# Optimization experiments

Hardware: AMD Instinct MI355X
Metric: run time of the kernel (lower is better)

Reference implementation:

```python
import jax, jax.numpy as jnp
import numpy as np

B, N = 32, 2048
SLOTS, PSD, VIEW = 5, 15, 9
DM, NH, MH, EGO = 64, 4, 128, 32
PAIR_D = SLOTS * (SLOTS - 1) // 2          # 10
TER_D = VIEW * VIEW                        # 81
NBR_D = SLOTS * PSD + PAIR_D               # 85
D_OBS = EGO + NBR_D + TER_D                # 198


def setup_inputs() -> dict:
    key = jax.random.key(0)
    ks = jax.random.split(key, 64)

    def _p(k, shape, s=0.05):
        return (jax.random.normal(k, shape) * s).astype(jnp.float32)

    def z(*shape):
        return jnp.zeros(shape, jnp.float32)

    # --- observation with some genuinely-masked slots (r == 0) ---
    ego = jax.random.normal(ks[0], (B, N, EGO), jnp.float32)
    nbr = jax.random.normal(ks[1], (B, N, SLOTS, PSD), jnp.float32)
    keep = jax.random.bernoulli(ks[2], 0.8, (B, N, SLOTS)).astype(jnp.float32)
    nbr = jnp.concatenate([nbr[..., 0:3] * keep[..., None], nbr[..., 3:]], axis=-1)
    pair = jax.random.normal(ks[3], (B, N, PAIR_D), jnp.float32)
    ter = jax.random.normal(ks[4], (B, N, TER_D), jnp.float32)
    obs = jnp.concatenate([ego, nbr.reshape(B, N, SLOTS * PSD), pair, ter], axis=-1)

    i = 5
    def nk():
        nonlocal i
        i += 1
        return ks[i - 1]

    params = {
        "tok_w": _p(nk(), (12, DM)), "tok_b": z(DM),
        "ln1_s": jnp.ones((DM,), jnp.float32), "ln1_b": z(DM),
        "a1_qw": _p(nk(), (DM, DM)), "a1_qb": z(DM),
        "a1_kw": _p(nk(), (DM, DM)), "a1_kb": z(DM),
        "a1_vw": _p(nk(), (DM, DM)), "a1_vb": z(DM),
        "a1_ow": _p(nk(), (DM, DM)), "a1_ob": z(DM),
        "ln2_s": jnp.ones((DM,), jnp.float32), "ln2_b": z(DM),
        "m1_w": _p(nk(), (DM, MH)), "m1_b": z(MH),
        "m2_w": _p(nk(), (MH, MH)), "m2_b": z(MH),
        "m3_w": _p(nk(), (MH, DM)), "m3_b": z(DM),
        "e1_w": _p(nk(), (EGO, MH)), "e1_b": z(MH),
        "e2_w": _p(nk(), (MH, MH)), "e2_b": z(MH),
        "e3_w": _p(nk(), (MH, DM)), "e3_b": z(DM),
        "l1_w": _p(nk(), (2 * DM, MH)), "l1_b": z(MH),
        "l2_w": _p(nk(), (MH, MH)), "l2_b": z(MH),
        "l3_w": _p(nk(), (MH, 1)), "l3_b": z(1),
        "seed": _p(nk(), (1, 1, DM), 0.02),
        "p_qw": _p(nk(), (DM, DM)), "p_qb": z(DM),
        "p_kw": _p(nk(), (DM, DM)), "p_kb": z(DM),
        "p_vw": _p(nk(), (DM, DM)), "p_vb": z(DM),
        "p_ow": _p(nk(), (DM, DM)), "p_ob": z(DM),
        "pr_w": _p(nk(), (PAIR_D, DM)), "pr_b": z(DM),
        "h1_w": _p(nk(), (EGO + 2 * DM, MH)), "h1_b": z(MH),
        "h2_w": _p(nk(), (MH, MH)), "h2_b": z(MH),
        "h3_w": _p(nk(), (MH, MH)), "h3_b": z(MH),
    }
    return {"obs": obs, **params}


def _layernorm(x, s, b, eps=1e-6):
    m = jnp.mean(x, axis=-1, keepdims=True)
    v = jnp.var(x, axis=-1, keepdims=True)
    return (x - m) * jax.lax.rsqrt(v + eps) * s + b


def _zero_if_masked(x, mask):
    return jnp.where(mask[..., None], x, jnp.array(0.0, x.dtype))


def _masked_softmax(logits, mask, eps=1e-9):
    mask = mask.astype(bool)
    very_neg = jnp.array(-1e9, logits.dtype)
    ml = jnp.where(mask, logits, very_neg)
    mx = jnp.max(ml, axis=-1, keepdims=True)
    ex = jnp.exp(ml - mx) * mask.astype(logits.dtype)
    return ex / (jnp.sum(ex, axis=-1, keepdims=True) + eps)


def _mha(q_in, kv_in, attn_mask, qw, qb, kw, kb, vw, vb, ow, ob, nh=NH):
    dm = q_in.shape[-1]
    dh = dm // nh
    q = (q_in @ qw + qb).reshape(*q_in.shape[:-1], nh, dh)
    k = (kv_in @ kw + kb).reshape(*kv_in.shape[:-1], nh, dh)
    v = (kv_in @ vw + vb).reshape(*kv_in.shape[:-1], nh, dh)
    logits = jnp.einsum('...qhd,...khd->...hqk', q, k) / jnp.sqrt(jnp.float32(dh))
    neg = jnp.finfo(logits.dtype).min
    logits = jnp.where(attn_mask, logits, neg)
    attn = jax.nn.softmax(logits, axis=-1)
    o = jnp.einsum('...hqk,...khd->...qhd', attn, v).reshape(*q_in.shape[:-1], dm)
    return o @ ow + ob


def _mlp3(x, w1, b1, w2, b2, w3, b3):
    x = jax.nn.gelu(x @ w1 + b1)
    x = jax.nn.gelu(x @ w2 + b2)
    return x @ w3 + b3


def reference(obs, tok_w, tok_b, ln1_s, ln1_b,
              a1_qw, a1_qb, a1_kw, a1_kb, a1_vw, a1_vb, a1_ow, a1_ob,
              ln2_s, ln2_b, m1_w, m1_b, m2_w, m2_b, m3_w, m3_b,
              e1_w, e1_b, e2_w, e2_b, e3_w, e3_b,
              l1_w, l1_b, l2_w, l2_b, l3_w, l3_b,
              seed, p_qw, p_qb, p_kw, p_kb, p_vw, p_vb, p_ow, p_ob,
              pr_w, pr_b, h1_w, h1_b, h2_w, h2_b, h3_w, h3_b):
    obs = obs.astype(jnp.float32)
    Bb, Nn, Dd = obs.shape
    ego = obs[..., :EGO]
    nbr_all = obs[..., EGO:EGO + NBR_D]
    nbr_main = nbr_all[..., :SLOTS * PSD].reshape(Bb, Nn, SLOTS, PSD)
    pair = nbr_all[..., SLOTS * PSD:]

    r = nbr_main[..., 0:3]
    u = nbr_main[..., 3:6]
    att = nbr_main[..., 6:9]
    fre = nbr_main[..., 9:10]
    tem = nbr_main[..., 10:11]
    inv = nbr_main[..., 11:15]

    mask = jnp.any(jnp.abs(r) > 1e-6, axis=-1)                 # (B,N,K)
    mask_any = jnp.any(mask, axis=-1, keepdims=True)           # (B,N,1)
    mask_safe = jnp.where(mask_any, mask, mask.at[..., 0].set(True))

    r_clean = jnp.nan_to_num(r, nan=0.0, posinf=0.0, neginf=0.0)
    diff = r_clean[..., :, None, :] - r_clean[..., None, :, :]
    dist = jnp.linalg.norm(diff, axis=-1)                      # (B,N,K,K)
    pair_mask = mask[..., :, None] & mask[..., None, :]
    eye = jnp.eye(SLOTS, dtype=bool)[None, None]
    valid = pair_mask & ~eye
    big = jnp.array(1e9, dist.dtype)
    dist_no_self = jnp.where(eye, big, dist)
    d_min = jnp.min(jnp.where(valid, dist_no_self, big), axis=-1, keepdims=True)
    d_sum = jnp.sum(jnp.where(valid, dist, 0.0), axis=-1, keepdims=True)
    cnt = jnp.sum(valid, axis=-1, keepdims=True).astype(dist.dtype)
    d_mean = jnp.where(cnt > 0, d_sum / (cnt + 1e-9), 0.0)
    att_norm = jnp.linalg.norm(att, axis=-1, keepdims=True)

    tok_in = jnp.concatenate([inv, fre, tem, att, att_norm, d_min, d_mean], axis=-1)  # (B,N,K,12)
    tok = jax.nn.gelu(tok_in @ tok_w + tok_b)
    tok = _zero_if_masked(tok, mask)

    # --- SetTransformerBlock ---
    qk = mask_safe[..., :, None] & mask_safe[..., None, :]
    attn_mask = qk[..., None, :, :]                            # (B,N,1,K,K)
    y = _layernorm(tok, ln1_s, ln1_b)
    y = _mha(y, y, attn_mask, a1_qw, a1_qb, a1_kw, a1_kb, a1_vw, a1_vb, a1_ow, a1_ob)
    y = _zero_if_masked(y, mask)
    tok = tok + y
    zz = _layernorm(tok, ln2_s, ln2_b)
    zz = _mlp3(zz, m1_w, m1_b, m2_w, m2_b, m3_w, m3_b)
    zz = _zero_if_masked(zz, mask)
    tok = _zero_if_masked(tok + zz, mask)

    # --- alpha weights ---
    ego_ctx = _mlp3(ego, e1_w, e1_b, e2_w, e2_b, e3_w, e3_b)   # (B,N,DM)
    ego_ctx_b = jnp.broadcast_to(ego_ctx[..., None, :], tok.shape)
    logits = _mlp3(jnp.concatenate([tok, ego_ctx_b], axis=-1),
                   l1_w, l1_b, l2_w, l2_b, l3_w, l3_b)[..., 0]
    alpha = _masked_softmax(logits, mask)
    alpha3 = alpha[..., None]
    v_r = jnp.sum(alpha3 * r, axis=-2)
    v_u = jnp.sum(alpha3 * u, axis=-2)

    # --- AttentionPool ---
    q = jnp.broadcast_to(seed, (*tok.shape[:-2], 1, DM)).astype(jnp.float32)
    pool_mask = mask_safe[..., None, None, :]                  # (B,N,1,1,K)
    c = _mha(q, tok, pool_mask, p_qw, p_qb, p_kw, p_kb, p_vw, p_vb, p_ow, p_ob)[..., 0, :]
    c = jnp.where(mask_any, c, jnp.zeros_like(c))

    pair_emb = jax.nn.gelu(pair @ pr_w + pr_b)
    h_in = jnp.concatenate([ego, c, pair_emb], axis=-1)
    h = _mlp3(h_in, h1_w, h1_b, h2_w, h2_b, h3_w, h3_b)
    return jnp.concatenate([h, v_r, v_u], axis=-1)             # (B,N,134)
```

## Files before the change

### kernel.cpp

```cpp
#include <hip/hip_runtime.h>
#include <math.h>


#define DOBS 198
#define NEG_INF_F (-3.402823466e38f)

#define BAR() do { asm volatile("s_waitcnt lgkmcnt(0)" ::: "memory"); \
                   __builtin_amdgcn_s_barrier(); } while(0)

typedef __bf16 v8bf __attribute__((ext_vector_type(8)));
typedef __bf16 v4bf __attribute__((ext_vector_type(4)));
typedef float  v4f  __attribute__((ext_vector_type(4)));

struct P {
  const float *obs,*tok_w,*tok_b,*ln1_s,*ln1_b,
    *a1_qw,*a1_qb,*a1_kw,*a1_kb,*a1_vw,*a1_vb,*a1_ow,*a1_ob,
    *ln2_s,*ln2_b,*m1_w,*m1_b,*m2_w,*m2_b,*m3_w,*m3_b,
    *e1_w,*e1_b,*e2_w,*e2_b,*e3_w,*e3_b,
    *l1_w,*l1_b,*l2_w,*l2_b,*l3_w,*l3_b,
    *seed,*p_qw,*p_qb,*p_kw,*p_kb,*p_vw,*p_vb,*p_ow,*p_ob,
    *pr_w,*pr_b,*h1_w,*h1_b,*h2_w,*h2_b,*h3_w,*h3_b;
  float* out;
};
static_assert(sizeof(P) == 51*sizeof(void*), "P layout");

#define W_A1Q 0
#define W_A1K 4096
#define W_A1V 8192
#define W_A1O 12288
#define W_M1  16384
#define W_M2  24576
#define W_M3  40960
#define W_E1  49152
#define W_E2  53248
#define W_E3  69632
#define W_L1  77824
#define W_L2  94208
#define W_PK  110592
#define W_PV  114688
#define W_PO  118784
#define W_H1  122880
#define W_H2  143360
#define W_H3  159744
#define W_END 176128
#define W_QP  176128

__global__ __launch_bounds__(256)
void prep_w(P a, __bf16* ws)
{
  if (blockIdx.x == 172){
    int t = threadIdx.x;
    if (t < 64){
      float acc = a.p_qb[t];
      for (int k=0;k<64;k++) acc += a.seed[k]*a.p_qw[k*64+t];
      ((float*)(ws + W_QP))[t] = acc;
    }
    return;
  }
  const float* srcs[18] = {a.a1_qw,a.a1_kw,a.a1_vw,a.a1_ow,a.m1_w,a.m2_w,a.m3_w,
                           a.e1_w,a.e2_w,a.e3_w,a.l1_w,a.l2_w,a.p_kw,a.p_vw,a.p_ow,
                           a.h1_w,a.h2_w,a.h3_w};
  const int Ks[18]   = {64,64,64,64,64,128,128,32,128,128,128,128,64,64,64,160,128,128};
  const int Ns[18]   = {64,64,64,64,128,128,64,128,128,64,128,128,64,64,64,128,128,128};
  const int offs[18] = {W_A1Q,W_A1K,W_A1V,W_A1O,W_M1,W_M2,W_M3,W_E1,W_E2,W_E3,
                        W_L1,W_L2,W_PK,W_PV,W_PO,W_H1,W_H2,W_H3};
  __shared__ float tile[32][33];
  int b = blockIdx.x, m = 0, acc = 0;
  for (; m < 18; m++){
    int t = (Ks[m]/32)*(Ns[m]/32);
    if (b < acc + t) break;
    acc += t;
  }
  int lt = b - acc, K = Ks[m], N = Ns[m];
  int ntile = N/32, kt = lt/ntile, nt = lt%ntile;
  int tx = threadIdx.x & 31, ty = threadIdx.x >> 5;
  const float* S = srcs[m];
  #pragma unroll
  for (int rr=0; rr<32; rr+=8)
    tile[ty+rr][tx] = S[(size_t)(kt*32+ty+rr)*N + nt*32+tx];
  __syncthreads();
  __bf16* D = ws + offs[m];
  #pragma unroll
  for (int rr=0; rr<32; rr+=8)
    D[(size_t)(nt*32+ty+rr)*K + kt*32+tx] = (__bf16)tile[tx][ty+rr];
}

__device__ __forceinline__ float gelu_f(float x){
  float t = x * fmaf(0.0356774081f, x*x, 0.7978845608f);
  float u = __builtin_amdgcn_exp2f(-2.885390082f * t);
  return x * __builtin_amdgcn_rcpf(1.0f + u);
}

__device__ __forceinline__ void load16f(const __bf16* p, float* f){
  v8bf a = *(const v8bf*)p, b = *(const v8bf*)(p+8);
  #pragma unroll
  for (int i=0;i<8;i++){ f[i]=(float)a[i]; f[8+i]=(float)b[i]; }
}

template<int KT,int NTPW> struct WF {
  v8bf  w[NTPW][KT];
  float4 b[NTPW];
};

template<int KT,int NTPW>
__device__ __forceinline__ WF<KT,NTPW> wload(const __bf16* __restrict__ Wt,
    const float* __restrict__ bias, int wv, int lane)
{
  WF<KT,NTPW> f;
  const int ar = lane&15, quad = lane>>4;
  #pragma unroll
  for (int ln=0; ln<NTPW; ln++){
    const int wt = wv*NTPW + ln;
    const __bf16* wp = Wt + (size_t)(wt*16+ar)*(KT*32) + quad*8;
    #pragma unroll
    for (int kt=0;kt<KT;kt++) f.w[ln][kt] = *(const v8bf*)(wp + kt*32);
    f.b[ln] = *(const float4*)(bias + wt*16 + quad*4);
  }
  return f;
}

template<int KT,int MT,int NTPW,typename LA,typename E>
__device__ __forceinline__ void gemmW(LA la, const WF<KT,NTPW>& f,
    int wv, int lane, E epi)
{
  const int ar = lane&15, quad = lane>>4;
  #pragma unroll
  for (int ln=0; ln<NTPW; ln++){
    const int wt = wv*NTPW + ln;
    #pragma unroll
    for (int mt=0; mt<MT; mt++){
      v4f c; c[0]=f.b[ln].x; c[1]=f.b[ln].y; c[2]=f.b[ln].z; c[3]=f.b[ln].w;
      #pragma unroll
      for (int kt=0;kt<KT;kt++)
        c = __builtin_amdgcn_mfma_f32_16x16x32_bf16(f.w[ln][kt], la(mt,kt,ar,quad), c, 0,0,0);
      epi(wt*16 + quad*4, mt, ar, c);
    }
  }
}

__global__ __launch_bounds__(256,3)
void swarm_mfma(P a, const __bf16* __restrict__ ws, int ntok)
{
  __shared__ char smem[53120] __attribute__((aligned(16)));
  __bf16* Ab   = (__bf16*)(smem);
  __bf16* Bb   = (__bf16*)(smem+17408);
  float*  TOKIN= (float*) (smem+17408);
  __bf16* Tk   = (__bf16*)(smem+34816);
  float*  OBSf = (float*) (smem+34816);
  __bf16* Po   = (__bf16*)(smem+34816);
  __bf16* Pe   = (__bf16*)(smem+44032);
  __bf16* Eg   = (__bf16*)(smem+46080);
  __bf16* Ru   = (__bf16*)(smem+47360);
  __bf16* mfb  = (__bf16*)(smem+48096);
  __bf16* msfb = (__bf16*)(smem+48224);
  float*  many = (float*) (smem+48352);
  float*  lga  = (float*) (smem+48416);
  __bf16* ECX  = (__bf16*)(smem+48672);
  float*  pattn= (float*) (smem+48672);
  __bf16* ATTb = (__bf16*)(smem+50720);
  __bf16* Cc   = (__bf16*)(smem+50720);

  const int lane = threadIdx.x & 63;
  const int wv   = threadIdx.x >> 6;
  const int ar   = lane & 15, quad = lane >> 4;
  const long blkT0 = (long)blockIdx.x*12;

  for (int it=lane; it<3*117; it+=64){
    int tg=it/117, c=it-tg*117;
    long gt = blkT0 + 3*wv + tg; if (gt>ntok-1) gt=ntok-1;
    OBSf[(3*wv+tg)*120+c] = a.obs[gt*DOBS+c];
  }
  float* Df = (float*)Ab;
  for (int it=lane; it<75; it+=64){
    int tg=it/25, p=it-tg*25, i=p/5, j=p-i*5;
    const float* ob = OBSf + (3*wv+tg)*120 + 32;
    float d2=0.f;
    #pragma unroll
    for (int d=0;d<3;d++){
      float ri=ob[15*i+d]; ri = isfinite(ri)?ri:0.f;
      float rj=ob[15*j+d]; rj = isfinite(rj)?rj:0.f;
      float df=ri-rj; d2 += df*df;
    }
    Df[(3*wv+tg)*32+p]=sqrtf(d2);
  }
  if (lane<15){
    int T=3*wv+lane/5, s=lane%5;
    const float* b = OBSf + T*120 + 32 + 15*s;
    mfb[15*wv+lane] = (__bf16)((fabsf(b[0])>1e-6f||fabsf(b[1])>1e-6f||fabsf(b[2])>1e-6f)?1.f:0.f);
  }
  if (wv==0 && lane>=60){ mfb[lane]=(__bf16)0.f; msfb[lane]=(__bf16)0.f; }
  if (wv==0 && lane>=12 && lane<16) many[lane]=0.f;
  if (lane<3){
    int T=3*wv+lane;
    float any = (float)mfb[T*5]+(float)mfb[T*5+1]+(float)mfb[T*5+2]+(float)mfb[T*5+3]+(float)mfb[T*5+4];
    float anyf = (any>0.f)?1.f:0.f; many[T]=anyf;
    #pragma unroll
    for (int i=0;i<5;i++) msfb[T*5+i] = (anyf>0.f)? mfb[T*5+i] : (__bf16)((i==0)?1.f:0.f);
  }
  if (lane<15){
    int T=3*wv+lane/5, i=lane%5, R=15*wv+lane;
    float dmin=1e9f,dsum=0.f,cnt=0.f;
    #pragma unroll
    for (int j=0;j<5;j++){
      if (j!=i && (float)mfb[T*5+i]>0.5f && (float)mfb[T*5+j]>0.5f){
        float dd=Df[T*32+i*5+j];
        dmin=fminf(dmin,dd); dsum+=dd; cnt+=1.f;
      }
    }
    TOKIN[R*12+10]=dmin;
    TOKIN[R*12+11]=(cnt>0.f)? dsum/(cnt+1e-9f) : 0.f;
  }
  for (int it=lane; it<150; it+=64){
    int tg=it/50, q=it-tg*50, s=q/10, c=q-s*10;
    int T=3*wv+tg;
    const float* b = OBSf + T*120 + 32 + 15*s;
    float v;
    if (c<4)        v=b[11+c];
    else if (c==4)  v=b[9];
    else if (c==5)  v=b[10];
    else if (c<9)   v=b[6+(c-6)];
    else { float a0=b[6],a1=b[7],a2=b[8]; v=sqrtf(a0*a0+a1*a1+a2*a2); }
    TOKIN[(T*5+s)*12+c]=v;
  }
  for (int it=lane; it<96; it+=64){
    int tg=it>>5, c=it&31;
    Eg[(3*wv+tg)*40+c] = (__bf16)OBSf[(3*wv+tg)*120+c];
  }
  for (int it=lane; it<90; it+=64){
    int tg=it/30, c=it-tg*30;
    Ru[(3*wv+tg)*30+c] = (__bf16)OBSf[(3*wv+tg)*120+32+15*(c/6)+(c%6)];
  }
  for (int it=lane; it<192; it+=64){
    int tg=it>>6, c=it&63;
    float acc = a.pr_b[c];
    #pragma unroll
    for (int k=0;k<10;k++) acc += OBSf[(3*wv+tg)*120+107+k]*a.pr_w[k*64+c];
    Pe[(3*wv+tg)*64+c] = (__bf16)gelu_f(acc);
  }
  BAR();

  auto wfK = wload<2,1>(ws+W_A1K, a.a1_kb, wv, lane);

  {
    float w0[12];
    #pragma unroll
    for (int k=0;k<12;k++) w0[k] = a.tok_w[k*64+lane];
    float tb = a.tok_b[lane];
    for (int r=0;r<15;r++){
      int R = 15*wv + r;
      const float4* tin = (const float4*)(TOKIN + R*12);
      float4 x0 = tin[0], x1 = tin[1], x2 = tin[2];
      float acc = tb;
      acc=fmaf(x0.x,w0[0],acc); acc=fmaf(x0.y,w0[1],acc);
      acc=fmaf(x0.z,w0[2],acc); acc=fmaf(x0.w,w0[3],acc);
      acc=fmaf(x1.x,w0[4],acc); acc=fmaf(x1.y,w0[5],acc);
      acc=fmaf(x1.z,w0[6],acc); acc=fmaf(x1.w,w0[7],acc);
      acc=fmaf(x2.x,w0[8],acc); acc=fmaf(x2.y,w0[9],acc);
      acc=fmaf(x2.z,w0[10],acc); acc=fmaf(x2.w,w0[11],acc);
      Tk[R*72+lane] = (__bf16)(gelu_f(acc)*(float)mfb[R]);
    }
  }
  if (ar<15){
    int R = 15*wv + ar;
    float x[16]; load16f(Tk + R*72 + quad*16, x);
    float s=0.f;
    #pragma unroll
    for (int i=0;i<16;i++) s += x[i];
    s += __shfl_xor(s,16,64); s += __shfl_xor(s,32,64);
    float m = s*(1.f/64.f), q=0.f;
    #pragma unroll
    for (int i=0;i<16;i++){ float d=x[i]-m; q=fmaf(d,d,q); }
    q += __shfl_xor(q,16,64); q += __shfl_xor(q,32,64);
    float rs = __builtin_amdgcn_rsqf(q*(1.f/64.f)+1e-6f);
    v8bf o0,o1;
    #pragma unroll
    for (int i=0;i<8;i++){
      o0[i]=(__bf16)((x[i]  -m)*rs*a.ln1_s[quad*16+i]  +a.ln1_b[quad*16+i]);
      o1[i]=(__bf16)((x[8+i]-m)*rs*a.ln1_s[quad*16+8+i]+a.ln1_b[quad*16+8+i]);
    }
    *(v8bf*)(Ab+R*136+quad*16)=o0; *(v8bf*)(Ab+R*136+quad*16+8)=o1;
  }
  BAR();

  auto actAb = [&](int mt,int kt,int r,int q){ return *(const v8bf*)(Ab + (size_t)(mt*16+r)*136 + q*8 + kt*32); };
  auto actBb = [&](int mt,int kt,int r,int q){ return *(const v8bf*)(Bb + (size_t)(mt*16+r)*136 + q*8 + kt*32); };
  auto actTk = [&](int mt,int kt,int r,int q){ return *(const v8bf*)(Tk + (size_t)(mt*16+r)*72  + q*8 + kt*32); };

  auto wfV = wload<2,1>(ws+W_A1V, a.a1_vb, wv, lane);
  auto wfQ = wload<2,1>(ws+W_A1Q, a.a1_qb, wv, lane);
  gemmW<2,4,1>(actAb, wfK, wv, lane,
    [&](int wb,int mt,int r,v4f c){ v4bf o;
      #pragma unroll
      for (int k=0;k<4;k++) o[k]=(__bf16)c[k];
      *(v4bf*)&Bb[(mt*16+r)*136+64+wb]=o; });
  gemmW<2,4,1>(actAb, wfV, wv, lane,
    [&](int wb,int mt,int r,v4f c){ v4bf o;
      #pragma unroll
      for (int k=0;k<4;k++) o[k]=(__bf16)c[k];
      *(v4bf*)&Ab[(mt*16+r)*136+64+wb]=o; });
  gemmW<2,4,1>(actAb, wfQ, wv, lane,
    [&](int wb,int mt,int r,v4f c){ v4bf o;
      #pragma unroll
      for (int k=0;k<4;k++) o[k]=(__bf16)c[k];
      *(v4bf*)&Bb[(mt*16+r)*136+wb]=o; });
  auto wfO = wload<2,1>(ws+W_A1O, a.a1_ob, wv, lane);
  BAR();

  if (lane<60){
    int tg=lane/20, rem=lane-tg*20, h=rem/5, i=rem-h*5;
    int T=3*wv+tg;
    bool mi = (float)msfb[T*5+i]>0.5f;
    float qv[16]; load16f(&Bb[(T*5+i)*136 + h*16], qv);
    float lgv[5], mx=NEG_INF_F;
    #pragma unroll
    for (int j=0;j<5;j++){
      float kk[16]; load16f(&Bb[(T*5+j)*136 + 64 + h*16], kk);
      float d=0.f;
      #pragma unroll
      for (int dd=0;dd<16;dd++) d += qv[dd]*kk[dd];
      bool mj = (float)msfb[T*5+j]>0.5f;
      lgv[j] = (mi&&mj)? d*0.25f : NEG_INF_F;
      mx = fmaxf(mx,lgv[j]);
    }
    float sum=0.f, ex[5];
    #pragma unroll
    for (int j=0;j<5;j++){ ex[j]=__expf(lgv[j]-mx); sum+=ex[j]; }
    float inv=1.0f/sum;
    #pragma unroll
    for (int j=0;j<5;j++) ATTb[T*100+(h*5+i)*5+j]=(__bf16)(ex[j]*inv);
  }
  {
    int h = lane>>4;
    #pragma unroll
    for (int tg=0; tg<3; tg++){
      int T=3*wv+tg;
      float v5[5];
      #pragma unroll
      for (int j=0;j<5;j++) v5[j] = (float)Ab[(T*5+j)*136+64+lane];
      #pragma unroll
      for (int i=0;i<5;i++){
        float o=0.f;
        #pragma unroll
        for (int j=0;j<5;j++) o += (float)ATTb[T*100+(h*5+i)*5+j]*v5[j];
        Ab[(T*5+i)*136+lane]=(__bf16)o;
      }
    }
  }
  BAR();

  gemmW<2,4,1>(actAb, wfO, wv, lane,
    [&](int wb,int mt,int r,v4f c){
      int R=mt*16+r; float mm=(float)mfb[R];
      v4bf old=*(const v4bf*)&Tk[R*72+wb]; v4bf o;
      #pragma unroll
      for (int k=0;k<4;k++) o[k]=(__bf16)((float)old[k]+c[k]*mm);
      *(v4bf*)&Tk[R*72+wb]=o; });
  auto wfM1 = wload<2,2>(ws+W_M1, a.m1_b, wv, lane);
  BAR();

  if (ar<15){
    int R = 15*wv + ar;
    float x[16]; load16f(Tk + R*72 + quad*16, x);
    float s=0.f;
    #pragma unroll
    for (int i=0;i<16;i++) s += x[i];
    s += __shfl_xor(s,16,64); s += __shfl_xor(s,32,64);
    float m = s*(1.f/64.f), q=0.f;
    #pragma unroll
    for (int i=0;i<16;i++){ float d=x[i]-m; q=fmaf(d,d,q); }
    q += __shfl_xor(q,16,64); q += __shfl_xor(q,32,64);
    float rs = __builtin_amdgcn_rsqf(q*(1.f/64.f)+1e-6f);
    v8bf o0,o1;
    #pragma unroll
    for (int i=0;i<8;i++){
      o0[i]=(__bf16)((x[i]  -m)*rs*a.ln2_s[quad*16+i]  +a.ln2_b[quad*16+i]);
      o1[i]=(__bf16)((x[8+i]-m)*rs*a.ln2_s[quad*16+8+i]+a.ln2_b[quad*16+8+i]);
    }
    *(v8bf*)(Ab+R*136+quad*16)=o0; *(v8bf*)(Ab+R*136+quad*16+8)=o1;
  }
  BAR();

  gemmW<2,4,2>(actAb, wfM1, wv, lane,
    [&](int wb,int mt,int r,v4f c){ v4bf o;
      #pragma unroll
      for (int k=0;k<4;k++) o[k]=(__bf16)gelu_f(c[k]);
      *(v4bf*)&Bb[(mt*16+r)*136+wb]=o; });
  auto wfM2 = wload<4,2>(ws+W_M2, a.m2_b, wv, lane);
  BAR();
  gemmW<4,4,2>(actBb, wfM2, wv, lane,
    [&](int wb,int mt,int r,v4f c){ v4bf o;
      #pragma unroll
      for (int k=0;k<4;k++) o[k]=(__bf16)gelu_f(c[k]);
      *(v4bf*)&Ab[(mt*16+r)*136+wb]=o; });
  auto wfM3 = wload<4,1>(ws+W_M3, a.m3_b, wv, lane);
  auto wfE1 = wload<1,2>(ws+W_E1, a.e1_b, wv, lane);
  BAR();
  gemmW<4,4,1>(actAb, wfM3, wv, lane,
    [&](int wb,int mt,int r,v4f c){
      int R=mt*16+r; float mm=(float)mfb[R];
      v4bf old=*(const v4bf*)&Tk[R*72+wb]; v4bf o;
      #pragma unroll
      for (int k=0;k<4;k++) o[k]=(__bf16)(((float)old[k]+c[k]*mm)*mm);
      *(v4bf*)&Tk[R*72+wb]=o; });
  gemmW<1,1,2>([&](int,int,int r,int q){ return *(const v8bf*)(Eg + (size_t)r*40 + q*8); },
    wfE1, wv, lane,
    [&](int wb,int mt,int r,v4f c){ v4bf o;
      #pragma unroll
      for (int k=0;k<4;k++) o[k]=(__bf16)gelu_f(c[k]);
      *(v4bf*)&Bb[r*136+wb]=o; });
  auto wfE2 = wload<4,2>(ws+W_E2, a.e2_b, wv, lane);
  BAR();
  gemmW<4,1,2>(actBb, wfE2, wv, lane,
    [&](int wb,int mt,int r,v4f c){ v4bf o;
      #pragma unroll
      for (int k=0;k<4;k++) o[k]=(__bf16)gelu_f(c[k]);
      *(v4bf*)&Ab[r*136+wb]=o; });
  auto wfE3 = wload<4,1>(ws+W_E3, a.e3_b, wv, lane);
  BAR();
  gemmW<4,1,1>(actAb, wfE3, wv, lane,
    [&](int wb,int mt,int r,v4f c){ v4bf o;
      #pragma unroll
      for (int k=0;k<4;k++) o[k]=(__bf16)c[k];
      *(v4bf*)&ECX[r*64+wb]=o; });
  auto wfL1 = wload<4,2>(ws+W_L1, a.l1_b, wv, lane);
  BAR();
  gemmW<4,4,2>([&](int mt,int kt,int r,int q){
      int R=mt*16+r;
      return (kt<2) ? *(const v8bf*)(Tk + (size_t)R*72 + q*8 + kt*32)
                    : *(const v8bf*)(ECX + (size_t)((R*205)>>10)*64 + q*8 + (kt-2)*32); },
    wfL1, wv, lane,
    [&](int wb,int mt,int r,v4f c){ v4bf o;
      #pragma unroll
      for (int k=0;k<4;k++) o[k]=(__bf16)gelu_f(c[k]);
      *(v4bf*)&Bb[(mt*16+r)*136+wb]=o; });
  auto wfL2 = wload<4,2>(ws+W_L2, a.l2_b, wv, lane);
  BAR();
  gemmW<4,4,2>(actBb, wfL2, wv, lane,
    [&](int wb,int mt,int r,v4f c){ v4bf o;
      #pragma unroll
      for (int k=0;k<4;k++) o[k]=(__bf16)gelu_f(c[k]);
      *(v4bf*)&Ab[(mt*16+r)*136+wb]=o; });
  auto wfPK = wload<2,1>(ws+W_PK, a.p_kb, wv, lane);
  auto wfPV = wload<2,1>(ws+W_PV, a.p_vb, wv, lane);
  BAR();

  if (ar<15){
    int R = 15*wv + ar;
    float x[16], y[16];
    load16f(&Ab[R*136 + quad*32], x);
    load16f(&Ab[R*136 + quad*32 + 16], y);
    const float* w = a.l3_w + quad*32;
    float p = 0.f;
    #pragma unroll
    for (int i=0;i<16;i++) p = fmaf(x[i], w[i], p);
    #pragma unroll
    for (int i=0;i<16;i++) p = fmaf(y[i], w[16+i], p);
    p += __shfl_xor(p,16,64); p += __shfl_xor(p,32,64);
    if (quad==0) lga[R] = p + a.l3_b[0];
  }
  gemmW<2,4,1>(actTk, wfPK, wv, lane,
    [&](int wb,int mt,int r,v4f c){ v4bf o;
      #pragma unroll
      for (int k=0;k<4;k++) o[k]=(__bf16)c[k];
      *(v4bf*)&Bb[(mt*16+r)*136+wb]=o; });
  gemmW<2,4,1>(actTk, wfPV, wv, lane,
    [&](int wb,int mt,int r,v4f c){ v4bf o;
      #pragma unroll
      for (int k=0;k<4;k++) o[k]=(__bf16)c[k];
      *(v4bf*)&Bb[(mt*16+r)*136+64+wb]=o; });
  if (lane<3){
    int T=3*wv+lane;
    float ml[5], mx=-1e9f;
    #pragma unroll
    for (int i=0;i<5;i++){ ml[i]=((float)mfb[T*5+i]>0.5f)? lga[T*5+i] : -1e9f; mx=fmaxf(mx,ml[i]); }
    float den=0.f, e[5];
    #pragma unroll
    for (int i=0;i<5;i++){ e[i]=__expf(ml[i]-mx)*(float)mfb[T*5+i]; den+=e[i]; }
    float inv=1.0f/(den+1e-9f);
    #pragma unroll
    for (int i=0;i<5;i++) lga[T*5+i]=e[i]*inv;
  }
  if (lane<18){
    int tg=lane/6, c=lane-tg*6;
    int T=3*wv+tg;
    float v=0.f;
    #pragma unroll
    for (int i=0;i<5;i++) v += lga[T*5+i]*(float)Ru[T*30+i*6+c];
    long tk = blkT0 + T;
    if (tk<ntok) a.out[tk*134+128+c]=v;
  }
  BAR();

  if (lane<12){
    const float* qg = (const float*)(ws + W_QP);
    int tg=lane>>2, h=lane&3;
    int T=3*wv+tg;
    float qv[16];
    #pragma unroll
    for (int dd=0;dd<16;dd++) qv[dd]=qg[h*16+dd];
    float lgv[5], mx=NEG_INF_F;
    #pragma unroll
    for (int j=0;j<5;j++){
      float kk[16]; load16f(&Bb[(T*5+j)*136 + h*16], kk);
      float d=0.f;
      #pragma unroll
      for (int dd=0;dd<16;dd++) d += qv[dd]*kk[dd];
      lgv[j] = ((float)msfb[T*5+j]>0.5f)? d*0.25f : NEG_INF_F;
      mx = fmaxf(mx,lgv[j]);
    }
    float sum=0.f, ex[5];
    #pragma unroll
    for (int j=0;j<5;j++){ ex[j]=__expf(lgv[j]-mx); sum+=ex[j]; }
    float inv=1.0f/sum;
    #pragma unroll
    for (int j=0;j<5;j++) pattn[T*20+h*5+j]=ex[j]*inv;
  }
  for (int it=lane; it<192; it+=64){
    int tg=it>>6, c=it&63, h=c>>4;
    int T=3*wv+tg;
    float o=0.f;
    #pragma unroll
    for (int j=0;j<5;j++)
      o += pattn[T*20+h*5+j]*(float)Bb[(T*5+j)*136+64+c];
    Po[T*64+c]=(__bf16)o;
  }
  auto wfPO = wload<2,1>(ws+W_PO, a.p_ob, wv, lane);
  BAR();

  gemmW<2,1,1>([&](int,int kt,int r,int q){ return *(const v8bf*)(Po + (size_t)r*64 + q*8 + kt*32); },
    wfPO, wv, lane,
    [&](int wb,int mt,int r,v4f c){
      float mm = many[r];
      v4bf o;
      #pragma unroll
      for (int k=0;k<4;k++) o[k]=(__bf16)(c[k]*mm);
      *(v4bf*)&Cc[r*64+wb]=o; });
  auto wfH1 = wload<5,2>(ws+W_H1, a.h1_b, wv, lane);
  BAR();

  gemmW<5,1,2>([&](int,int kt,int r,int q){
      if (kt==0) return *(const v8bf*)(Eg + (size_t)r*40 + q*8);
      if (kt<3)  return *(const v8bf*)(Cc + (size_t)r*64 + q*8 + (kt-1)*32);
      return *(const v8bf*)(Pe + (size_t)r*64 + q*8 + (kt-3)*32); },
    wfH1, wv, lane,
    [&](int wb,int mt,int r,v4f c){ v4bf o;
      #pragma unroll
      for (int k=0;k<4;k++) o[k]=(__bf16)gelu_f(c[k]);
      *(v4bf*)&Bb[r*136+wb]=o; });
  auto wfH2 = wload<4,2>(ws+W_H2, a.h2_b, wv, lane);
  BAR();
  gemmW<4,1,2>(actBb, wfH2, wv, lane,
    [&](int wb,int mt,int r,v4f c){ v4bf o;
      #pragma unroll
      for (int k=0;k<4;k++) o[k]=(__bf16)gelu_f(c[k]);
      *(v4bf*)&Ab[r*136+wb]=o; });
  auto wfH3 = wload<4,2>(ws+W_H3, a.h3_b, wv, lane);
  BAR();
  gemmW<4,1,2>(actAb, wfH3, wv, lane,
    [&](int wb,int mt,int r,v4f c){
      long tk = blkT0 + r;
      if (r<12 && tk<ntok){
        float2* o2 = (float2*)&a.out[tk*134 + wb];
        o2[0] = make_float2(c[0], c[1]);
        o2[1] = make_float2(c[2], c[3]);
      } });
}

extern "C" void kernel_launch(void* const* d_in, const int* in_sizes, int n_in,
                              void* d_out, int out_size, void* d_ws, size_t ws_size,
                              hipStream_t stream)
{
  P a;
  const float** pp = reinterpret_cast<const float**>(&a);
  for (int i=0;i<50;i++) pp[i] = reinterpret_cast<const float*>(d_in[i]);
  a.out = reinterpret_cast<float*>(d_out);
  int ntok = in_sizes[0] / DOBS;

  __bf16* ws = reinterpret_cast<__bf16*>(d_ws);
  hipLaunchKernelGGL(prep_w, dim3(173), dim3(256), 0, stream, a, ws);
  hipLaunchKernelGGL(swarm_mfma, dim3((ntok+11)/12), dim3(256), 0, stream, a, ws, ntok);
}
```

Measured before the change: 497.9 us.

## Fuse attention output projection with LayerNorm2 via per-wave row ownership

The attention output projection is restructured so each wave computes a 16-row M-tile across all four N-tiles instead of one N-tile across all rows. With that ownership the residual add and LayerNorm2 run in registers right after the MFMAs, which drops one barrier and a round trip of the token rows through LDS. Rows 60-63 of the token buffer are now zeroed because each wave's tile covers 16 rows instead of 15. In exchange each wave loads the full output-projection weight, which adds register pressure.

New measurement: 499.9 us. About the same (+0.4%).

```diff
diff --git a/kernel.cpp b/kernel.cpp
--- a/kernel.cpp
+++ b/kernel.cpp
@@ -115,6 +115,22 @@
     #pragma unroll
     for (int kt=0;kt<KT;kt++) f.w[ln][kt] = *(const v8bf*)(wp + kt*32);
     f.b[ln] = *(const float4*)(bias + wt*16 + quad*4);
+  }
+  return f;
+}
+
+template<int KT,int NT>
+__device__ __forceinline__ WF<KT,NT> wloadA(const __bf16* __restrict__ Wt,
+    const float* __restrict__ bias, int lane)
+{
+  WF<KT,NT> f;
+  const int ar = lane&15, quad = lane>>4;
+  #pragma unroll
+  for (int ln=0; ln<NT; ln++){
+    const __bf16* wp = Wt + (size_t)(ln*16+ar)*(KT*32) + quad*8;
+    #pragma unroll
+    for (int kt=0;kt<KT;kt++) f.w[ln][kt] = *(const v8bf*)(wp + kt*32);
+    f.b[ln] = *(const float4*)(bias + ln*16 + quad*4);
   }
   return f;
 }
@@ -183,6 +199,9 @@
     }
     Df[(3*wv+tg)*32+p]=sqrtf(d2);
   }
+  if (wv==1){
+    for (int it=lane; it<288; it+=64) Tk[60*72+it] = (__bf16)0.f;
+  }
   if (lane<15){
     int T=3*wv+lane/5, s=lane%5;
     const float* b = OBSf + T*120 + 32 + 15*s;
@@ -303,7 +322,6 @@
       #pragma unroll
       for (int k=0;k<4;k++) o[k]=(__bf16)c[k];
       *(v4bf*)&Bb[(mt*16+r)*136+wb]=o; });
-  auto wfO = wload<2,1>(ws+W_A1O, a.a1_ob, wv, lane);
   BAR();
 
   if (lane<60){
@@ -346,38 +364,56 @@
       }
     }
   }
-  BAR();
-
-  gemmW<2,4,1>(actAb, wfO, wv, lane,
-    [&](int wb,int mt,int r,v4f c){
-      int R=mt*16+r; float mm=(float)mfb[R];
-      v4bf old=*(const v4bf*)&Tk[R*72+wb]; v4bf o;
-      #pragma unroll
-      for (int k=0;k<4;k++) o[k]=(__bf16)((float)old[k]+c[k]*mm);
-      *(v4bf*)&Tk[R*72+wb]=o; });
-  auto wfM1 = wload<2,2>(ws+W_M1, a.m1_b, wv, lane);
-  BAR();
-
-  if (ar<15){
-    int R = 15*wv + ar;
-    float x[16]; load16f(Tk + R*72 + quad*16, x);
+  auto wfO = wloadA<2,4>(ws+W_A1O, a.a1_ob, lane);
+  BAR();
+
+  {
+    float4 s2[4], b2[4];
+    #pragma unroll
+    for (int nt=0; nt<4; nt++){
+      s2[nt] = *(const float4*)(a.ln2_s + nt*16 + quad*4);
+      b2[nt] = *(const float4*)(a.ln2_b + nt*16 + quad*4);
+    }
+    const int R = wv*16 + ar;
+    const float mm = (float)mfb[R];
+    float acc[16];
+    #pragma unroll
+    for (int nt=0; nt<4; nt++){
+      v4f c; c[0]=wfO.b[nt].x; c[1]=wfO.b[nt].y; c[2]=wfO.b[nt].z; c[3]=wfO.b[nt].w;
+      #pragma unroll
+      for (int kt=0; kt<2; kt++)
+        c = __builtin_amdgcn_mfma_f32_16x16x32_bf16(wfO.w[nt][kt], actAb(wv,kt,ar,quad), c, 0,0,0);
+      v4bf old = *(const v4bf*)&Tk[R*72 + nt*16 + quad*4];
+      #pragma unroll
+      for (int k=0;k<4;k++) acc[nt*4+k] = (float)old[k] + c[k]*mm;
+    }
+    #pragma unroll
+    for (int nt=0; nt<4; nt++){
+      v4bf o;
+      #pragma unroll
+      for (int k=0;k<4;k++) o[k] = (__bf16)acc[nt*4+k];
+      *(v4bf*)&Tk[R*72 + nt*16 + quad*4] = o;
+    }
     float s=0.f;
     #pragma unroll
-    for (int i=0;i<16;i++) s += x[i];
+    for (int i=0;i<16;i++) s += acc[i];
     s += __shfl_xor(s,16,64); s += __shfl_xor(s,32,64);
     float m = s*(1.f/64.f), q=0.f;
     #pragma unroll
-    for (int i=0;i<16;i++){ float d=x[i]-m; q=fmaf(d,d,q); }
+    for (int i=0;i<16;i++){ float d=acc[i]-m; q=fmaf(d,d,q); }
     q += __shfl_xor(q,16,64); q += __shfl_xor(q,32,64);
     float rs = __builtin_amdgcn_rsqf(q*(1.f/64.f)+1e-6f);
-    v8bf o0,o1;
-    #pragma unroll
-    for (int i=0;i<8;i++){
-      o0[i]=(__bf16)((x[i]  -m)*rs*a.ln2_s[quad*16+i]  +a.ln2_b[quad*16+i]);
-      o1[i]=(__bf16)((x[8+i]-m)*rs*a.ln2_s[quad*16+8+i]+a.ln2_b[quad*16+8+i]);
-    }
-    *(v8bf*)(Ab+R*136+quad*16)=o0; *(v8bf*)(Ab+R*136+quad*16+8)=o1;
-  }
+    #pragma unroll
+    for (int nt=0; nt<4; nt++){
+      v4bf o;
+      o[0]=(__bf16)((acc[nt*4+0]-m)*rs*s2[nt].x+b2[nt].x);
+      o[1]=(__bf16)((acc[nt*4+1]-m)*rs*s2[nt].y+b2[nt].y);
+      o[2]=(__bf16)((acc[nt*4+2]-m)*rs*s2[nt].z+b2[nt].z);
+      o[3]=(__bf16)((acc[nt*4+3]-m)*rs*s2[nt].w+b2[nt].w);
+      *(v4bf*)&Ab[R*136 + nt*16 + quad*4] = o;
+    }
+  }
+  auto wfM1 = wload<2,2>(ws+W_M1, a.m1_b, wv, lane);
   BAR();
 
   gemmW<2,4,2>(actAb, wfM1, wv, lane,
```
